# Kernel optimization log

Hardware: AMD Instinct MI355X
Metric: run time of the kernel (lower is better)

The kernel has to match this reference:

```python
import jax, jax.numpy as jnp
import numpy as np

EMB = 1024
HEADS = 16
HEAD_DIM = EMB // HEADS


def setup_inputs() -> dict:
    key = jax.random.key(0)
    ks = jax.random.split(key, 9)
    s = 1.0 / np.sqrt(EMB)
    x = jax.random.normal(ks[0], (4, 2048, EMB), dtype=jnp.float32)
    Wq = jax.random.uniform(ks[1], (EMB, EMB), minval=-s, maxval=s, dtype=jnp.float32)
    bq = jax.random.uniform(ks[2], (EMB,), minval=-s, maxval=s, dtype=jnp.float32)
    Wk = jax.random.uniform(ks[3], (EMB, EMB), minval=-s, maxval=s, dtype=jnp.float32)
    bk = jax.random.uniform(ks[4], (EMB,), minval=-s, maxval=s, dtype=jnp.float32)
    Wv = jax.random.uniform(ks[5], (EMB, EMB), minval=-s, maxval=s, dtype=jnp.float32)
    bv = jax.random.uniform(ks[6], (EMB,), minval=-s, maxval=s, dtype=jnp.float32)
    Wo = jax.random.uniform(ks[7], (EMB, EMB), minval=-s, maxval=s, dtype=jnp.float32)
    bo = jax.random.uniform(ks[8], (EMB,), minval=-s, maxval=s, dtype=jnp.float32)
    return {"x": x, "Wq": Wq, "bq": bq, "Wk": Wk, "bk": bk, "Wv": Wv, "bv": bv, "Wo": Wo, "bo": bo}


def reference(x, Wq, bq, Wk, bk, Wv, bv, Wo, bo):
    B, S, E = x.shape
    # QKV projections (torch Linear: y = x W^T + b)
    q = x @ Wq.T + bq
    k = x @ Wk.T + bk
    v = x @ Wv.T + bv
    # split heads -> [B, H, S, Dh]
    q = q.reshape(B, S, HEADS, HEAD_DIM).transpose(0, 2, 1, 3)
    k = k.reshape(B, S, HEADS, HEAD_DIM).transpose(0, 2, 1, 3)
    v = v.reshape(B, S, HEADS, HEAD_DIM).transpose(0, 2, 1, 3)
    # NOTE: module scales by 1/sqrt(emb_size), NOT 1/sqrt(head_dim)
    scale = 1.0 / jnp.sqrt(jnp.asarray(E, dtype=x.dtype))
    energy = jnp.einsum('bhqd,bhkd->bhqk', q, k) * scale
    attention = jax.nn.softmax(energy, axis=-1)
    out = jnp.einsum('bhqk,bhkd->bhqd', attention, v)
    out = out.transpose(0, 2, 1, 3).reshape(B, S, E)
    return out @ Wo.T + bo
```

## Files before the change

### kernel.cpp

```cpp
#include <hip/hip_runtime.h>


typedef __bf16 bf16;
typedef __attribute__((ext_vector_type(4))) short shortx4;
typedef __attribute__((ext_vector_type(8))) short short8;
typedef __attribute__((ext_vector_type(4))) float floatx4;
typedef __attribute__((ext_vector_type(2))) unsigned int uintx2;
typedef __attribute__((ext_vector_type(4))) unsigned int uintx4;

#define MFMA16(a, b, c) __builtin_amdgcn_mfma_f32_16x16x32_bf16((a), (b), (c), 0, 0, 0)

#define LDS_STRIDE 56

__device__ __forceinline__ float fast_exp2(float x) {
    float r;
    asm("v_exp_f32 %0, %1" : "=v"(r) : "v"(x));
    return r;
}
__device__ __forceinline__ unsigned int cvt_pk_bf16(float lo, float hi) {
    unsigned int r;
    asm("v_cvt_pk_bf16_f32 %0, %1, %2" : "=v"(r) : "v"(lo), "v"(hi));
    return r;
}

__device__ __forceinline__ void async16(const bf16* __restrict__ g, short* l) {
    __builtin_amdgcn_global_load_lds((const __attribute__((address_space(1))) void*)g,
                                     (__attribute__((address_space(3))) void*)l, 16, 0, 0);
}

__device__ __forceinline__ short8 frag8(const bf16* __restrict__ p) {
    return *(const short8*)p;
}
__device__ __forceinline__ short8 frag8(const float* __restrict__ p) {
    const floatx4 a = *(const floatx4*)p;
    const floatx4 b = *(const floatx4*)(p + 4);
    short8 r;
#pragma unroll
    for (int j = 0; j < 4; j++) {
        r[j]     = __builtin_bit_cast(short, (bf16)a[j]);
        r[4 + j] = __builtin_bit_cast(short, (bf16)b[j]);
    }
    return r;
}

__global__ __launch_bounds__(256) void to_bf16(
    const float* __restrict__ in, bf16* __restrict__ out, int n8)
{
    const int i = blockIdx.x * 256 + threadIdx.x;
    if (i >= n8) return;
    const floatx4 a = *(const floatx4*)(in + (size_t)i * 8);
    const floatx4 b = *(const floatx4*)(in + (size_t)i * 8 + 4);
    short8 r;
#pragma unroll
    for (int j = 0; j < 4; j++) {
        r[j]     = __builtin_bit_cast(short, (bf16)a[j]);
        r[4 + j] = __builtin_bit_cast(short, (bf16)b[j]);
    }
    *(short8*)((short*)out + (size_t)i * 8) = r;
}

__global__ __launch_bounds__(256) void to_bf16_w4(
    const float* __restrict__ Wq, const float* __restrict__ Wk,
    const float* __restrict__ Wv, const float* __restrict__ Wo,
    bf16* __restrict__ out)
{
    const int i = blockIdx.x * 256 + threadIdx.x;
    const int t = i >> 17;
    const int j = i & 131071;
    const float* src = (t == 0) ? Wq : (t == 1) ? Wk : (t == 2) ? Wv : Wo;
    const floatx4 a = *(const floatx4*)(src + (size_t)j * 8);
    const floatx4 b = *(const floatx4*)(src + (size_t)j * 8 + 4);
    short8 r;
#pragma unroll
    for (int jj = 0; jj < 4; jj++) {
        r[jj]     = __builtin_bit_cast(short, (bf16)a[jj]);
        r[4 + jj] = __builtin_bit_cast(short, (bf16)b[jj]);
    }
    *(short8*)((short*)out + (size_t)t * 1048576 + (size_t)j * 8) = r;
}

__device__ __forceinline__ void gemm128_p3(
    const bf16* __restrict__ A, const bf16* __restrict__ B,
    int m0, int n0, short* As, short* Bs, floatx4 acc[4][4])
{
    const int tid  = threadIdx.x;
    const int lane = tid & 63;
    const int w    = tid >> 6;
    const int wu   = __builtin_amdgcn_readfirstlane(w);
    const int wm   = w >> 1, wn = w & 1;
    const int g    = lane >> 4, c = lane & 15;
    const int ar   = lane >> 2;
    const int aq   = ((lane & 3) ^ (ar & 3)) * 8;
    const int aswz = (g ^ (c & 3)) * 8;

#pragma unroll
    for (int mi = 0; mi < 4; mi++)
#pragma unroll
        for (int ni = 0; ni < 4; ni++)
            acc[mi][ni] = (floatx4){0.f, 0.f, 0.f, 0.f};

    const bf16* Arow0 = A + (size_t)(m0 + w * 32 + ar) * 1024 + aq;
    const bf16* Arow1 = A + (size_t)(m0 + w * 32 + 16 + ar) * 1024 + aq;
    const bf16* Brow0 = B + (size_t)(n0 + w * 32 + ar) * 1024 + aq;
    const bf16* Brow1 = B + (size_t)(n0 + w * 32 + 16 + ar) * 1024 + aq;

    {
        short* Ad = As + wu * 1024;
        short* Bd = Bs + wu * 1024;
        async16(Arow0, Ad);        async16(Arow1, Ad + 512);
        async16(Brow0, Bd);        async16(Brow1, Bd + 512);
        async16(Arow0 + 32, Ad + 4096);  async16(Arow1 + 32, Ad + 4096 + 512);
        async16(Brow0 + 32, Bd + 4096);  async16(Brow1 + 32, Bd + 4096 + 512);
    }

    int cur = 0;
    for (int t = 0; t < 32; ++t) {
        if (t < 31) asm volatile("s_waitcnt vmcnt(4)" ::: "memory");
        else        asm volatile("s_waitcnt vmcnt(0)" ::: "memory");
        __builtin_amdgcn_sched_barrier(0);
        __builtin_amdgcn_s_barrier();
        __builtin_amdgcn_sched_barrier(0);

        const short* Ac = As + cur * 4096;
        const short* Bc = Bs + cur * 4096;
        short8 af[4], bfr[4];
#pragma unroll
        for (int mi = 0; mi < 4; mi++)
            af[mi] = *(const short8*)(Ac + (wm * 64 + mi * 16 + c) * 32 + aswz);
#pragma unroll
        for (int ni = 0; ni < 4; ni++)
            bfr[ni] = *(const short8*)(Bc + (wn * 64 + ni * 16 + c) * 32 + aswz);
#pragma unroll
        for (int mi = 0; mi < 4; mi++)
#pragma unroll
            for (int ni = 0; ni < 4; ni++)
                acc[mi][ni] = MFMA16(af[mi], bfr[ni], acc[mi][ni]);

        if (t < 30) {
            const int kn  = (t + 2) * 32;
            const int nb  = (cur == 0) ? 2 : cur - 1;
            short* Ad = As + nb * 4096 + wu * 1024;
            short* Bd = Bs + nb * 4096 + wu * 1024;
            async16(Arow0 + kn, Ad);   async16(Arow1 + kn, Ad + 512);
            async16(Brow0 + kn, Bd);   async16(Brow1 + kn, Bd + 512);
        }
        cur = (cur == 2) ? 0 : cur + 1;
    }
}

__device__ __forceinline__ void gemm128_fallback(
    const bf16* __restrict__ A, const float* __restrict__ B,
    int m0, int n0, short* As, short* Bs, floatx4 acc[4][4])
{
    const int tid  = threadIdx.x;
    const int lane = tid & 63;
    const int w    = tid >> 6;
    const int wu   = __builtin_amdgcn_readfirstlane(w);
    const int wm   = w >> 1, wn = w & 1;
    const int g    = lane >> 4, c = lane & 15;
    const int ar = lane >> 2;
    const int aq = ((lane & 3) ^ (ar & 3)) * 8;
    const int lrow = tid >> 2;
    const int lc8  = (tid & 3) * 8;

#pragma unroll
    for (int mi = 0; mi < 4; mi++)
#pragma unroll
        for (int ni = 0; ni < 4; ni++)
            acc[mi][ni] = (floatx4){0.f, 0.f, 0.f, 0.f};

    const int aswz = (g ^ (c & 3)) * 8;

    for (int k0 = 0; k0 < 1024; k0 += 32) {
        async16(A + (size_t)(m0 + w * 32 + ar) * 1024 + k0 + aq,      As + wu * 1024);
        async16(A + (size_t)(m0 + w * 32 + 16 + ar) * 1024 + k0 + aq, As + wu * 1024 + 512);
        *(short8*)(Bs + lrow * LDS_STRIDE + lc8) =
            frag8(B + (size_t)(n0 + lrow) * 1024 + k0 + lc8);
        *(short8*)(Bs + (lrow + 64) * LDS_STRIDE + lc8) =
            frag8(B + (size_t)(n0 + lrow + 64) * 1024 + k0 + lc8);
        __syncthreads();

        short8 af[4], bfr[4];
#pragma unroll
        for (int mi = 0; mi < 4; mi++)
            af[mi] = *(const short8*)(As + (wm * 64 + mi * 16 + c) * 32 + aswz);
#pragma unroll
        for (int ni = 0; ni < 4; ni++)
            bfr[ni] = *(const short8*)(Bs + (wn * 64 + ni * 16 + c) * LDS_STRIDE + g * 8);
#pragma unroll
        for (int mi = 0; mi < 4; mi++)
#pragma unroll
            for (int ni = 0; ni < 4; ni++)
                acc[mi][ni] = MFMA16(af[mi], bfr[ni], acc[mi][ni]);
        __syncthreads();
    }
}

template <typename TB>
__global__ __launch_bounds__(256) void qkv_gemm(
    const bf16* __restrict__ Xb,
    const TB* __restrict__ Wq, const TB* __restrict__ Wk, const TB* __restrict__ Wv,
    const float* __restrict__ bq, const float* __restrict__ bk, const float* __restrict__ bv,
    bf16* __restrict__ qkv)
{
    __shared__ __align__(16) short As[(sizeof(TB) == 2) ? 12288 : 4096];
    __shared__ __align__(16) short Bs[(sizeof(TB) == 2) ? 12288 : 128 * LDS_STRIDE];

    const int z = blockIdx.z;
    const TB* W       = (z == 0) ? Wq : (z == 1) ? Wk : Wv;
    const float* bias = (z == 0) ? bq : (z == 1) ? bk : bv;
    bf16* outz = qkv + (size_t)z * (8192u * 1024u);

    const int m0 = blockIdx.y * 128;
    const int n0 = blockIdx.x * 128;

    floatx4 acc[4][4];
    if constexpr (sizeof(TB) == 2)
        gemm128_p3(Xb, (const bf16*)W, m0, n0, As, Bs, acc);
    else
        gemm128_fallback(Xb, (const float*)W, m0, n0, As, Bs, acc);

    const int lane = threadIdx.x & 63;
    const int w = threadIdx.x >> 6;
    const int wm = w >> 1, wn = w & 1;
    const int g = lane >> 4, c = lane & 15;

    if (z == 2) {
#pragma unroll
        for (int ni = 0; ni < 4; ni++) {
            const int n = n0 + wn * 64 + ni * 16 + c;
            const float bb = bias[n];
            const int h = n >> 6, d = n & 63;
#pragma unroll
            for (int mi = 0; mi < 4; mi++) {
                const int m = m0 + wm * 64 + mi * 16 + g * 4;
                const int b = m >> 11, s = m & 2047;
                shortx4 st;
#pragma unroll
                for (int r = 0; r < 4; r++)
                    st[r] = __builtin_bit_cast(short, (bf16)(acc[mi][ni][r] + bb));
                *(shortx4*)&outz[(((size_t)((b << 4) | h)) * 64 + d) * 2048 + s] = st;
            }
        }
    } else {
#pragma unroll
        for (int ni = 0; ni < 4; ni++) {
            const int n = n0 + wn * 64 + ni * 16 + c;
            const float bb = bias[n];
            const int h = n >> 6, d = n & 63;
#pragma unroll
            for (int mi = 0; mi < 4; mi++) {
#pragma unroll
                for (int r = 0; r < 4; r++) {
                    const int m = m0 + wm * 64 + mi * 16 + g * 4 + r;
                    const int b = m >> 11, s = m & 2047;
                    outz[(((size_t)((b << 4) | h)) * 2048 + s) * 64 + d] =
                        (bf16)(acc[mi][ni][r] + bb);
                }
            }
        }
    }
}

__global__ __launch_bounds__(256, 2) void attn_kernel(
    const bf16* __restrict__ qkv, bf16* __restrict__ attn_out)
{
    __shared__ __align__(16) short Ks[2][128 * 64];
    __shared__ __align__(16) short Vs[2][64 * 128];

    const int linear = blockIdx.y * gridDim.x + blockIdx.x;
    const int slot = linear >> 3;
    const int bh = (linear & 7) * 8 + (slot >> 4);
    const int q0 = (slot & 15) * 128;

    const size_t HSTRIDE = 2048u * 64u;
    const bf16* __restrict__ Q  = qkv + (size_t)bh * HSTRIDE;
    const bf16* __restrict__ Kp = qkv + 8192u * 1024u + (size_t)bh * HSTRIDE;
    const bf16* __restrict__ Vt = qkv + 2u * 8192u * 1024u + (size_t)bh * HSTRIDE;

    const int tid  = threadIdx.x;
    const int lane = tid & 63;
    const int w    = tid >> 6;
    const int wu   = __builtin_amdgcn_readfirstlane(w);
    const int g    = lane >> 4, c = lane & 15;

    const float C2 = 0.04508422002778f;

    const int krow_off = lane >> 3;
    const int kchunk   = (lane & 7) ^ (lane >> 3);
    const int vrow_off = lane >> 4;

    short8 qf[2][2];
#pragma unroll
    for (int qb = 0; qb < 2; qb++)
#pragma unroll
        for (int ks = 0; ks < 2; ks++)
            qf[qb][ks] = *(const short8*)(Q + (size_t)(q0 + w * 32 + qb * 16 + c) * 64
                                            + ks * 32 + g * 8);

    floatx4 o[2][4];
#pragma unroll
    for (int mi = 0; mi < 2; mi++)
#pragma unroll
        for (int di = 0; di < 4; di++)
            o[mi][di] = (floatx4){0.f, 0.f, 0.f, 0.f};
    float m_run[2] = {-1e30f, -1e30f};
    float l_run[2] = {0.f, 0.f};

#pragma unroll
    for (int s = 0; s < 4; s++) {
        const int row = w * 32 + s * 8 + krow_off;
        async16(Kp + (size_t)row * 64 + kchunk * 8, &Ks[0][(wu * 32 + s * 8) * 64]);
    }
#pragma unroll
    for (int s = 0; s < 4; s++) {
        const int row = w * 16 + s * 4 + vrow_off;
        const int vchunk = (lane & 15) ^ (row & 15);
        async16(Vt + (size_t)row * 2048 + vchunk * 8, &Vs[0][(wu * 16 + s * 4) * 128]);
    }
    __syncthreads();

    int cur = 0;
    for (int kb = 0; kb < 16; kb++) {
        if (kb < 15) {
            const int kn = (kb + 1) * 128;
#pragma unroll
            for (int s = 0; s < 4; s++) {
                const int row = w * 32 + s * 8 + krow_off;
                async16(Kp + (size_t)(kn + row) * 64 + kchunk * 8,
                        &Ks[cur ^ 1][(wu * 32 + s * 8) * 64]);
            }
#pragma unroll
            for (int s = 0; s < 4; s++) {
                const int row = w * 16 + s * 4 + vrow_off;
                const int vchunk = (lane & 15) ^ (row & 15);
                async16(Vt + (size_t)row * 2048 + kn + vchunk * 8,
                        &Vs[cur ^ 1][(wu * 16 + s * 4) * 128]);
            }
        }

        const short* __restrict__ Kc = &Ks[cur][0];
        const short* __restrict__ Vc = &Vs[cur][0];

        floatx4 sAcc[2][8];
#pragma unroll
        for (int qb = 0; qb < 2; qb++)
#pragma unroll
            for (int ni = 0; ni < 8; ni++)
                sAcc[qb][ni] = (floatx4){0.f, 0.f, 0.f, 0.f};
#pragma unroll
        for (int ks = 0; ks < 2; ks++)
#pragma unroll
            for (int ni = 0; ni < 8; ni++) {
                const short8 kf = *(const short8*)(
                    Kc + (16 * ni + c) * 64 + (((ks * 4 + g) ^ (c & 7)) * 8));
                sAcc[0][ni] = MFMA16(kf, qf[0][ks], sAcc[0][ni]);
                sAcc[1][ni] = MFMA16(kf, qf[1][ks], sAcc[1][ni]);
            }

        float alpha[2];
        unsigned int lo[2][8], hi[2][8];
#pragma unroll
        for (int qb = 0; qb < 2; qb++) {
            floatx4 mv = sAcc[qb][0];
#pragma unroll
            for (int ni = 1; ni < 8; ni++)
#pragma unroll
                for (int r = 0; r < 4; r++) mv[r] = fmaxf(mv[r], sAcc[qb][ni][r]);
            float mx = fmaxf(fmaxf(mv[0], mv[1]), fmaxf(mv[2], mv[3]));
            mx = fmaxf(mx, __shfl_xor(mx, 16));
            mx = fmaxf(mx, __shfl_xor(mx, 32));
            const float mnew = fmaxf(m_run[qb], mx * C2);
            alpha[qb] = fast_exp2(m_run[qb] - mnew);
            m_run[qb] = mnew;

            floatx4 sv = {0.f, 0.f, 0.f, 0.f};
#pragma unroll
            for (int ni = 0; ni < 8; ni++) {
#pragma unroll
                for (int r = 0; r < 4; r++) {
                    const float p = fast_exp2(fmaf(sAcc[qb][ni][r], C2, -mnew));
                    sAcc[qb][ni][r] = p;
                    sv[r] += p;
                }
                lo[qb][ni] = cvt_pk_bf16(sAcc[qb][ni][0], sAcc[qb][ni][1]);
                hi[qb][ni] = cvt_pk_bf16(sAcc[qb][ni][2], sAcc[qb][ni][3]);
            }
            float sum = (sv[0] + sv[1]) + (sv[2] + sv[3]);
            sum += __shfl_xor(sum, 16);
            sum += __shfl_xor(sum, 32);
            l_run[qb] = l_run[qb] * alpha[qb] + sum;
        }

#pragma unroll
        for (int mi = 0; mi < 2; mi++)
#pragma unroll
            for (int r = 0; r < 4; r++) {
                const int src = (lane & 48) | (g * 4 + r);
                const float a = __shfl(alpha[mi], src);
#pragma unroll
                for (int di = 0; di < 4; di++) o[mi][di][r] *= a;
            }

#pragma unroll
        for (int t = 0; t < 4; t++) {
            const short8 pf0 = __builtin_bit_cast(short8,
                (uintx4){lo[0][2 * t], hi[0][2 * t], lo[0][2 * t + 1], hi[0][2 * t + 1]});
            const short8 pf1 = __builtin_bit_cast(short8,
                (uintx4){lo[1][2 * t], hi[1][2 * t], lo[1][2 * t + 1], hi[1][2 * t + 1]});
#pragma unroll
            for (int di = 0; di < 4; di++) {
                const int rowb = (16 * di + c) * 128 + 4 * (g & 1);
                const uintx2 vlo = *(const uintx2*)(
                    Vc + rowb + (((4 * t + (g >> 1)) ^ c) * 8));
                const uintx2 vhi = *(const uintx2*)(
                    Vc + rowb + (((4 * t + 2 + (g >> 1)) ^ c) * 8));
                const short8 vf = __builtin_bit_cast(short8,
                    (uintx4){vlo[0], vlo[1], vhi[0], vhi[1]});
                o[0][di] = MFMA16(pf0, vf, o[0][di]);
                o[1][di] = MFMA16(pf1, vf, o[1][di]);
            }
        }

        if (kb < 15) __syncthreads();
        cur ^= 1;
    }

    const int b = bh >> 4, h = bh & 15;
#pragma unroll
    for (int mi = 0; mi < 2; mi++) {
#pragma unroll
        for (int r = 0; r < 4; r++) {
            const int src = (lane & 48) | (g * 4 + r);
            const float linv = 1.0f / __shfl(l_run[mi], src);
            const int srow = q0 + w * 32 + mi * 16 + g * 4 + r;
#pragma unroll
            for (int di = 0; di < 4; di++) {
                attn_out[((size_t)(b * 2048 + srow)) * 1024 + h * 64 + di * 16 + c] =
                    (bf16)(o[mi][di][r] * linv);
            }
        }
    }
}

template <typename TB>
__global__ __launch_bounds__(256) void out_gemm(
    const bf16* __restrict__ A, const TB* __restrict__ Wo,
    const float* __restrict__ bo, float* __restrict__ C)
{
    __shared__ __align__(16) short As[(sizeof(TB) == 2) ? 12288 : 4096];
    __shared__ __align__(16) short Bs[(sizeof(TB) == 2) ? 12288 : 128 * LDS_STRIDE];

    const int m0 = blockIdx.y * 128;
    const int n0 = blockIdx.x * 128;

    floatx4 acc[4][4];
    if constexpr (sizeof(TB) == 2)
        gemm128_p3(A, (const bf16*)Wo, m0, n0, As, Bs, acc);
    else
        gemm128_fallback(A, (const float*)Wo, m0, n0, As, Bs, acc);

    const int lane = threadIdx.x & 63;
    const int w = threadIdx.x >> 6;
    const int wm = w >> 1, wn = w & 1;
    const int g = lane >> 4, c = lane & 15;

#pragma unroll
    for (int ni = 0; ni < 4; ni++) {
        const int n = n0 + wn * 64 + ni * 16 + c;
        const float bb = bo[n];
#pragma unroll
        for (int mi = 0; mi < 4; mi++) {
#pragma unroll
            for (int r = 0; r < 4; r++) {
                const int m = m0 + wm * 64 + mi * 16 + g * 4 + r;
                C[(size_t)m * 1024 + n] = acc[mi][ni][r] + bb;
            }
        }
    }
}

extern "C" void kernel_launch(void* const* d_in, const int* in_sizes, int n_in,
                              void* d_out, int out_size, void* d_ws, size_t ws_size,
                              hipStream_t stream)
{
    const float* x  = (const float*)d_in[0];
    const float* Wq = (const float*)d_in[1];
    const float* bq = (const float*)d_in[2];
    const float* Wk = (const float*)d_in[3];
    const float* bk = (const float*)d_in[4];
    const float* Wv = (const float*)d_in[5];
    const float* bv = (const float*)d_in[6];
    const float* Wo = (const float*)d_in[7];
    const float* bo = (const float*)d_in[8];
    float* out = (float*)d_out;

    bf16* qkv  = (bf16*)d_ws;
    bf16* attn = qkv + 3u * 8192u * 1024u;
    bf16* xb   = attn;

    const size_t base = 64u * 1024u * 1024u;
    const bool haveW = ws_size >= base + 8u * 1024u * 1024u;
    bf16* wb = (bf16*)((char*)d_ws + base);

    to_bf16<<<dim3(4096), dim3(256), 0, stream>>>(x, xb, 1048576);

    if (haveW) {
        to_bf16_w4<<<dim3(2048), dim3(256), 0, stream>>>(Wq, Wk, Wv, Wo, wb);
        qkv_gemm<bf16><<<dim3(8, 64, 3), dim3(256), 0, stream>>>(
            xb, wb, wb + 1048576u, wb + 2u * 1048576u, bq, bk, bv, qkv);
    } else {
        qkv_gemm<float><<<dim3(8, 64, 3), dim3(256), 0, stream>>>(
            xb, Wq, Wk, Wv, bq, bk, bv, qkv);
    }

    attn_kernel<<<dim3(16, 64), dim3(256), 0, stream>>>(qkv, attn);

    if (haveW) {
        out_gemm<bf16><<<dim3(8, 64), dim3(256), 0, stream>>>(
            attn, wb + 3u * 1048576u, bo, out);
    } else {
        out_gemm<float><<<dim3(8, 64), dim3(256), 0, stream>>>(attn, Wo, bo, out);
    }
}
```

Before: 321.0 us.

## Use 512-thread attention blocks with 256 queries and remap GEMM block order for XCDs

The attention kernel now runs 8 waves per block covering 256 query rows, so each K/V tile loaded into LDS is shared by twice as many query rows. The cooperative async loads are re-split across 8 waves, and the grid is halved. The QKV and output GEMMs remap the linear block index so that consecutive blocks on the same XCD share A/B tiles in cache. The larger blocks reduce block count and may lower occupancy or create tail effects.

```diff
diff --git a/kernel.cpp b/kernel.cpp
--- a/kernel.cpp
+++ b/kernel.cpp
@@ -206,13 +206,16 @@
     __shared__ __align__(16) short As[(sizeof(TB) == 2) ? 12288 : 4096];
     __shared__ __align__(16) short Bs[(sizeof(TB) == 2) ? 12288 : 128 * LDS_STRIDE];
 
-    const int z = blockIdx.z;
+    const int lin = (blockIdx.z * 64 + blockIdx.y) * 8 + blockIdx.x;
+    const int wg  = (lin & 7) * 192 + (lin >> 3);
+    const int z   = wg >> 9;
+    const int rem = wg & 511;
+    const int m0  = (rem >> 3) * 128;
+    const int n0  = (rem & 7) * 128;
+
     const TB* W       = (z == 0) ? Wq : (z == 1) ? Wk : Wv;
     const float* bias = (z == 0) ? bq : (z == 1) ? bk : bv;
     bf16* outz = qkv + (size_t)z * (8192u * 1024u);
-
-    const int m0 = blockIdx.y * 128;
-    const int n0 = blockIdx.x * 128;
 
     floatx4 acc[4][4];
     if constexpr (sizeof(TB) == 2)
@@ -262,16 +265,16 @@
     }
 }
 
-__global__ __launch_bounds__(256, 2) void attn_kernel(
+__global__ __launch_bounds__(512, 4) void attn_kernel(
     const bf16* __restrict__ qkv, bf16* __restrict__ attn_out)
 {
     __shared__ __align__(16) short Ks[2][128 * 64];
     __shared__ __align__(16) short Vs[2][64 * 128];
 
-    const int linear = blockIdx.y * gridDim.x + blockIdx.x;
-    const int slot = linear >> 3;
-    const int bh = (linear & 7) * 8 + (slot >> 4);
-    const int q0 = (slot & 15) * 128;
+    const int lin  = blockIdx.y * gridDim.x + blockIdx.x;
+    const int slot = lin >> 3;
+    const int bh   = (lin & 7) * 8 + (slot >> 3);
+    const int q0   = (slot & 7) * 256;
 
     const size_t HSTRIDE = 2048u * 64u;
     const bf16* __restrict__ Q  = qkv + (size_t)bh * HSTRIDE;
@@ -289,6 +292,7 @@
     const int krow_off = lane >> 3;
     const int kchunk   = (lane & 7) ^ (lane >> 3);
     const int vrow_off = lane >> 4;
+    const int vchunk   = (lane & 15) ^ ((w * 4 + (lane >> 4)) & 15);
 
     short8 qf[2][2];
 #pragma unroll
@@ -308,15 +312,14 @@
     float l_run[2] = {0.f, 0.f};
 
 #pragma unroll
-    for (int s = 0; s < 4; s++) {
-        const int row = w * 32 + s * 8 + krow_off;
-        async16(Kp + (size_t)row * 64 + kchunk * 8, &Ks[0][(wu * 32 + s * 8) * 64]);
-    }
-#pragma unroll
-    for (int s = 0; s < 4; s++) {
-        const int row = w * 16 + s * 4 + vrow_off;
-        const int vchunk = (lane & 15) ^ (row & 15);
-        async16(Vt + (size_t)row * 2048 + vchunk * 8, &Vs[0][(wu * 16 + s * 4) * 128]);
+    for (int s = 0; s < 2; s++) {
+        const int row = s * 64 + w * 8 + krow_off;
+        async16(Kp + (size_t)row * 64 + kchunk * 8, &Ks[0][(s * 64 + wu * 8) * 64]);
+    }
+#pragma unroll
+    for (int s = 0; s < 2; s++) {
+        const int row = s * 32 + w * 4 + vrow_off;
+        async16(Vt + (size_t)row * 2048 + vchunk * 8, &Vs[0][(s * 32 + wu * 4) * 128]);
     }
     __syncthreads();
 
@@ -325,17 +328,16 @@
         if (kb < 15) {
             const int kn = (kb + 1) * 128;
 #pragma unroll
-            for (int s = 0; s < 4; s++) {
-                const int row = w * 32 + s * 8 + krow_off;
+            for (int s = 0; s < 2; s++) {
+                const int row = s * 64 + w * 8 + krow_off;
                 async16(Kp + (size_t)(kn + row) * 64 + kchunk * 8,
-                        &Ks[cur ^ 1][(wu * 32 + s * 8) * 64]);
-            }
-#pragma unroll
-            for (int s = 0; s < 4; s++) {
-                const int row = w * 16 + s * 4 + vrow_off;
-                const int vchunk = (lane & 15) ^ (row & 15);
+                        &Ks[cur ^ 1][(s * 64 + wu * 8) * 64]);
+            }
+#pragma unroll
+            for (int s = 0; s < 2; s++) {
+                const int row = s * 32 + w * 4 + vrow_off;
                 async16(Vt + (size_t)row * 2048 + kn + vchunk * 8,
-                        &Vs[cur ^ 1][(wu * 16 + s * 4) * 128]);
+                        &Vs[cur ^ 1][(s * 32 + wu * 4) * 128]);
             }
         }
 
@@ -451,8 +453,10 @@
     __shared__ __align__(16) short As[(sizeof(TB) == 2) ? 12288 : 4096];
     __shared__ __align__(16) short Bs[(sizeof(TB) == 2) ? 12288 : 128 * LDS_STRIDE];
 
-    const int m0 = blockIdx.y * 128;
-    const int n0 = blockIdx.x * 128;
+    const int lin = blockIdx.y * 8 + blockIdx.x;
+    const int wg  = (lin & 7) * 64 + (lin >> 3);
+    const int m0  = (wg >> 3) * 128;
+    const int n0  = (wg & 7) * 128;
 
     floatx4 acc[4][4];
     if constexpr (sizeof(TB) == 2)
@@ -514,7 +518,7 @@
             xb, Wq, Wk, Wv, bq, bk, bv, qkv);
     }
 
-    attn_kernel<<<dim3(16, 64), dim3(256), 0, stream>>>(qkv, attn);
+    attn_kernel<<<dim3(8, 64), dim3(512), 0, stream>>>(qkv, attn);
 
     if (haveW) {
         out_gemm<bf16><<<dim3(8, 64), dim3(256), 0, stream>>>(
```

Result: slower. 452.8 us (+41.0%).
